# Kernel tuning notes

Hardware: AMD Instinct MI355X
Metric: run time of the kernel (lower is better)

Reference implementation:

```python
import jax, jax.numpy as jnp
import numpy as np
import math

N = 100000
C = 128
E = 640000
ALPHA = 0.1
THETA = 1.0
LAYER = 4


def setup_inputs() -> dict:
    key = jax.random.key(0)
    k1, k2, k3, k4, k5, k6 = jax.random.split(key, 6)
    x = jax.random.normal(k1, (N, C), dtype=jnp.float32)
    x0 = jax.random.normal(k2, (N, C), dtype=jnp.float32)
    W = jax.random.normal(k3, (C, C), dtype=jnp.float32) / math.sqrt(C)
    b = jax.random.normal(k4, (C,), dtype=jnp.float32) * 0.01
    edge_index = jax.random.randint(k5, (2, E), 0, N, dtype=jnp.int64)
    return {"x": x, "x0": x0, "W": W, "b": b, "edge_index": edge_index}


def _symmetric_propagate(x, edge_index):
    n = x.shape[0]
    loop = jnp.arange(n, dtype=edge_index.dtype)
    src = jnp.concatenate([edge_index[0], loop])  # add self-loops (GCN norm)
    dst = jnp.concatenate([edge_index[1], loop])
    ones = jnp.ones(src.shape[0], dtype=x.dtype)
    deg = jax.ops.segment_sum(ones, dst, num_segments=n)
    dinv = jnp.where(deg > 0, jax.lax.rsqrt(deg), 0.0)
    norm = dinv[src] * dinv[dst]                  # [E+N]
    msgs = x[src] * norm[:, None]                 # gather + scale
    return jax.ops.segment_sum(msgs, dst, num_segments=n)  # scatter-add


def reference(x, x0, W, b, edge_index):
    propagated = _symmetric_propagate(x, edge_index)
    support = (1.0 - ALPHA) * propagated + ALPHA * x0
    beta = math.log(THETA / max(LAYER, 1) + 1.0)
    transformed = support @ W.T + b               # nn.Linear(channels, channels)
    return (1.0 - beta) * support + beta * transformed
```

## Files before the change

### kernel.cpp

```cpp
#include <hip/hip_runtime.h>
#include <stdint.h>

#define C 128
#define ALPHA_F 0.1f
#define ONE_MINUS_ALPHA 0.9f
#define BETA_F 0.22314355131420976f
#define ONE_MINUS_BETA 0.7768564486857902f

typedef __attribute__((ext_vector_type(8))) short bf16x8;
typedef __attribute__((ext_vector_type(4))) float f32x4;

__device__ inline float bf2f(unsigned short u) {
    union { unsigned int i; float f; } c;
    c.i = ((unsigned int)u) << 16;
    return c.f;
}
__device__ inline unsigned short f2bf(float f) {
    union { float f; unsigned int i; } c;
    c.f = f;
    unsigned int r = (c.i + 0x7FFFu + ((c.i >> 16) & 1u)) >> 16;
    return (unsigned short)r;
}

__global__ void k_init(const float* __restrict__ W, unsigned short* __restrict__ Vb,
                       int* __restrict__ cnt, int n) {
    int i = blockIdx.x * 256 + threadIdx.x;
    if (i < n) cnt[i] = 0;
    if (i < C * C) {
        int j = i >> 7;
        int c = i & 127;
        float v = BETA_F * W[i] + ((j == c) ? ONE_MINUS_BETA : 0.f);
        Vb[i] = f2bf(v);
    }
}

__global__ void k_hist(const int* __restrict__ dst, int* __restrict__ cnt,
                       int* __restrict__ rank, int e) {
    int i = blockIdx.x * blockDim.x + threadIdx.x;
    if (i < e) rank[i] = atomicAdd(&cnt[dst[i]], 1);
}

__global__ __launch_bounds__(256)
void k_scan_a(const int* __restrict__ cnt, int* __restrict__ part, int n) {
    __shared__ int s[256];
    int t = threadIdx.x;
    int i = blockIdx.x * 256 + t;
    s[t] = (i < n) ? cnt[i] : 0;
    __syncthreads();
    for (int off = 128; off > 0; off >>= 1) {
        if (t < off) s[t] += s[t + off];
        __syncthreads();
    }
    if (t == 0) part[blockIdx.x] = s[0];
}

__global__ __launch_bounds__(256)
void k_scan_bc(const int* __restrict__ cnt, const int* __restrict__ part,
               int4* __restrict__ meta, int* __restrict__ row_ptr,
               float* __restrict__ dinv, int n) {
    __shared__ int a[256];
    __shared__ int b[256];
    int t   = threadIdx.x;
    int bid = blockIdx.x;

    int local = 0;
    for (int k = t; k < bid; k += 256) local += part[k];
    a[t] = local;
    __syncthreads();
    for (int off = 128; off > 0; off >>= 1) {
        if (t < off) a[t] += a[t + off];
        __syncthreads();
    }
    int blockoff = a[0];
    __syncthreads();

    int i = bid * 256 + t;
    int v = (i < n) ? cnt[i] : 0;
    a[t] = v;
    __syncthreads();
    int* cur = a;
    int* nxt = b;
    for (int off = 1; off < 256; off <<= 1) {
        nxt[t] = cur[t] + ((t >= off) ? cur[t - off] : 0);
        __syncthreads();
        int* tmp = cur; cur = nxt; nxt = tmp;
    }
    if (i < n) {
        int rp = blockoff + cur[t] - v;
        float dv = rsqrtf((float)(v + 1));
        meta[i]    = make_int4(rp, v, __float_as_int(dv), 0);
        row_ptr[i] = rp;
        dinv[i]    = dv;
    }
}

__global__ void k_pl_ybf(const int* __restrict__ src, const int* __restrict__ dst,
                         const int* __restrict__ row_ptr, const int* __restrict__ rank,
                         int* __restrict__ sorted_src, int e,
                         const float* __restrict__ x, const float* __restrict__ dinv,
                         unsigned short* __restrict__ y, int n, int eb) {
    int bid = blockIdx.x;
    if (bid < eb) {
        int i = bid * 256 + threadIdx.x;
        if (i < e) {
            int d = dst[i];
            int pos = row_ptr[d] + rank[i];
            sorted_src[pos] = src[i];
        }
    } else {
        int t = (bid - eb) * 256 + threadIdx.x;
        int total = n * 32;
        if (t < total) {
            int i = t >> 5;
            float dv = dinv[i];
            float4 v = ((const float4*)x)[t];
            ushort4 o;
            o.x = f2bf(v.x * dv);
            o.y = f2bf(v.y * dv);
            o.z = f2bf(v.z * dv);
            o.w = f2bf(v.w * dv);
            ((ushort4*)y)[t] = o;
        }
    }
}

__global__ __launch_bounds__(256)
void k_gather(const unsigned short* __restrict__ y, const float* __restrict__ x0,
              const int* __restrict__ sorted_src, const int4* __restrict__ meta,
              float* __restrict__ soutf, unsigned short* __restrict__ soutb,
              int mode, int n) {
    int tid  = threadIdx.x;
    int l32  = tid & 31;
    int base = tid & 32;
    int node = blockIdx.x * 8 + (tid >> 5);
    if (node >= n) return;

    const ushort4* y4 = (const ushort4*)y;

    int4 md   = meta[node];
    int start = md.x;
    int len   = md.y;
    float dv  = __int_as_float(md.z);
    float4 xv = ((const float4*)x0)[(size_t)node * 32 + l32];

    int m = (len < 32) ? len : 32;
    int eidx = (l32 < m) ? sorted_src[start + l32] : node;

    bool b1 = 1 < m, b2 = 2 < m, b3 = 3 < m;
    bool b4 = 4 < m, b5 = 5 < m, b6 = 6 < m, b7 = 7 < m;
    int s0 = __shfl(eidx, base + 0, 64);
    int s1 = __shfl(eidx, base + (b1 ? 1 : 0), 64);
    int s2 = __shfl(eidx, base + (b2 ? 2 : 0), 64);
    int s3 = __shfl(eidx, base + (b3 ? 3 : 0), 64);
    int s4 = __shfl(eidx, base + (b4 ? 4 : 0), 64);
    int s5 = __shfl(eidx, base + (b5 ? 5 : 0), 64);
    int s6 = __shfl(eidx, base + (b6 ? 6 : 0), 64);
    int s7 = __shfl(eidx, base + (b7 ? 7 : 0), 64);
    ushort4 v0 = y4[(size_t)s0 * 32 + l32];
    ushort4 v1 = y4[(size_t)s1 * 32 + l32];
    ushort4 v2 = y4[(size_t)s2 * 32 + l32];
    ushort4 v3 = y4[(size_t)s3 * 32 + l32];
    ushort4 v4 = y4[(size_t)s4 * 32 + l32];
    ushort4 v5 = y4[(size_t)s5 * 32 + l32];
    ushort4 v6 = y4[(size_t)s6 * 32 + l32];
    ushort4 v7 = y4[(size_t)s7 * 32 + l32];
    ushort4 vs = y4[(size_t)node * 32 + l32];

    float w0 = (0 < m) ? 1.f : 0.f, w1 = b1 ? 1.f : 0.f, w2 = b2 ? 1.f : 0.f, w3 = b3 ? 1.f : 0.f;
    float w4 = b4 ? 1.f : 0.f, w5 = b5 ? 1.f : 0.f, w6 = b6 ? 1.f : 0.f, w7 = b7 ? 1.f : 0.f;

    float4 acc;
    acc.x = bf2f(vs.x) + w0 * bf2f(v0.x) + w1 * bf2f(v1.x) + w2 * bf2f(v2.x) + w3 * bf2f(v3.x)
                       + w4 * bf2f(v4.x) + w5 * bf2f(v5.x) + w6 * bf2f(v6.x) + w7 * bf2f(v7.x);
    acc.y = bf2f(vs.y) + w0 * bf2f(v0.y) + w1 * bf2f(v1.y) + w2 * bf2f(v2.y) + w3 * bf2f(v3.y)
                       + w4 * bf2f(v4.y) + w5 * bf2f(v5.y) + w6 * bf2f(v6.y) + w7 * bf2f(v7.y);
    acc.z = bf2f(vs.z) + w0 * bf2f(v0.z) + w1 * bf2f(v1.z) + w2 * bf2f(v2.z) + w3 * bf2f(v3.z)
                       + w4 * bf2f(v4.z) + w5 * bf2f(v5.z) + w6 * bf2f(v6.z) + w7 * bf2f(v7.z);
    acc.w = bf2f(vs.w) + w0 * bf2f(v0.w) + w1 * bf2f(v1.w) + w2 * bf2f(v2.w) + w3 * bf2f(v3.w)
                       + w4 * bf2f(v4.w) + w5 * bf2f(v5.w) + w6 * bf2f(v6.w) + w7 * bf2f(v7.w);

    for (int j = 8; j < m; j += 4) {
        bool c1 = (j + 1) < m, c2 = (j + 2) < m, c3 = (j + 3) < m;
        int t0 = __shfl(eidx, base + j, 64);
        int t1 = __shfl(eidx, base + (c1 ? j + 1 : j), 64);
        int t2 = __shfl(eidx, base + (c2 ? j + 2 : j), 64);
        int t3 = __shfl(eidx, base + (c3 ? j + 3 : j), 64);
        ushort4 u0 = y4[(size_t)t0 * 32 + l32];
        ushort4 u1 = y4[(size_t)t1 * 32 + l32];
        ushort4 u2 = y4[(size_t)t2 * 32 + l32];
        ushort4 u3 = y4[(size_t)t3 * 32 + l32];
        float q1 = c1 ? 1.f : 0.f, q2 = c2 ? 1.f : 0.f, q3 = c3 ? 1.f : 0.f;
        acc.x += bf2f(u0.x) + q1 * bf2f(u1.x) + q2 * bf2f(u2.x) + q3 * bf2f(u3.x);
        acc.y += bf2f(u0.y) + q1 * bf2f(u1.y) + q2 * bf2f(u2.y) + q3 * bf2f(u3.y);
        acc.z += bf2f(u0.z) + q1 * bf2f(u1.z) + q2 * bf2f(u2.z) + q3 * bf2f(u3.z);
        acc.w += bf2f(u0.w) + q1 * bf2f(u1.w) + q2 * bf2f(u2.w) + q3 * bf2f(u3.w);
    }

    for (int j = 32; j < len; ++j) {
        int t0 = sorted_src[start + j];
        ushort4 u0 = y4[(size_t)t0 * 32 + l32];
        acc.x += bf2f(u0.x);
        acc.y += bf2f(u0.y);
        acc.z += bf2f(u0.z);
        acc.w += bf2f(u0.w);
    }

    float4 s;
    s.x = ONE_MINUS_ALPHA * (dv * acc.x) + ALPHA_F * xv.x;
    s.y = ONE_MINUS_ALPHA * (dv * acc.y) + ALPHA_F * xv.y;
    s.z = ONE_MINUS_ALPHA * (dv * acc.z) + ALPHA_F * xv.z;
    s.w = ONE_MINUS_ALPHA * (dv * acc.w) + ALPHA_F * xv.w;

    if (mode) {
        unsigned long long pk =
            (unsigned long long)f2bf(s.x)
          | ((unsigned long long)f2bf(s.y) << 16)
          | ((unsigned long long)f2bf(s.z) << 32)
          | ((unsigned long long)f2bf(s.w) << 48);
        __builtin_nontemporal_store(
            pk, (unsigned long long*)(soutb + (size_t)node * C + l32 * 4));
    } else {
        ((float4*)soutf)[(size_t)node * 32 + l32] = s;
    }
}

__global__ __launch_bounds__(256)
void k_out(const float* __restrict__ sinf, const unsigned short* __restrict__ sinb,
           const unsigned short* __restrict__ Vb, const float* __restrict__ bias,
           float* __restrict__ out, int mode, int n) {
    __shared__ unsigned short wlds[128 * 128];
    __shared__ unsigned short slds[64 * 128];

    int tid  = threadIdx.x;
    int row0 = blockIdx.x * 64;

    const uint4* Vb16 = (const uint4*)Vb;
    for (int i = tid; i < 2048; i += 256) {
        int j = i >> 4;
        int g = i & 15;
        uint4 v = Vb16[i];
        *(uint4*)&wlds[j * 128 + (g ^ (j & 7)) * 8] = v;
    }

    if (mode) {
        const uint4* sb16 = (const uint4*)sinb;
        for (int i = tid; i < 1024; i += 256) {
            int r = i >> 4;
            int g = i & 15;
            int grow = row0 + r;
            uint4 v = make_uint4(0, 0, 0, 0);
            if (grow < n) v = sb16[(size_t)grow * 16 + g];
            *(uint4*)&slds[r * 128 + (g ^ (r & 7)) * 8] = v;
        }
    } else {
        for (int i = tid; i < 1024; i += 256) {
            int r = i >> 4;
            int g = i & 15;
            int grow = row0 + r;
            union { unsigned short u[8]; uint4 v; } pk;
            if (grow < n) {
                const float* p = sinf + (size_t)grow * C + g * 8;
                float4 aa = *(const float4*)p;
                float4 bb = *(const float4*)(p + 4);
                pk.u[0] = f2bf(aa.x); pk.u[1] = f2bf(aa.y);
                pk.u[2] = f2bf(aa.z); pk.u[3] = f2bf(aa.w);
                pk.u[4] = f2bf(bb.x); pk.u[5] = f2bf(bb.y);
                pk.u[6] = f2bf(bb.z); pk.u[7] = f2bf(bb.w);
            } else {
                pk.v = make_uint4(0, 0, 0, 0);
            }
            *(uint4*)&slds[r * 128 + (g ^ (r & 7)) * 8] = pk.v;
        }
    }
    __syncthreads();

    int w    = tid >> 6;
    int lane = tid & 63;
    int l16  = lane & 15;
    int h    = lane >> 4;
    int arow = w * 16 + l16;

    f32x4 acc[8];
    #pragma unroll
    for (int t = 0; t < 8; ++t) acc[t] = (f32x4){0.f, 0.f, 0.f, 0.f};

    #pragma unroll
    for (int k0 = 0; k0 < 128; k0 += 32) {
        int ga = ((k0 >> 3) + h) ^ (arow & 7);
        bf16x8 a = *(const bf16x8*)&slds[arow * 128 + ga * 8];
        #pragma unroll
        for (int t = 0; t < 8; ++t) {
            int brow = t * 16 + l16;
            int gb = ((k0 >> 3) + h) ^ (brow & 7);
            bf16x8 b = *(const bf16x8*)&wlds[brow * 128 + gb * 8];
            acc[t] = __builtin_amdgcn_mfma_f32_16x16x32_bf16(a, b, acc[t], 0, 0, 0);
        }
    }

    #pragma unroll
    for (int t = 0; t < 8; ++t) {
        int j  = t * 16 + l16;
        float bj = BETA_F * bias[j];
        #pragma unroll
        for (int e2 = 0; e2 < 4; ++e2) {
            int grow = row0 + w * 16 + h * 4 + e2;
            if (grow < n) {
                __builtin_nontemporal_store(acc[t][e2] + bj, &out[(size_t)grow * C + j]);
            }
        }
    }
}

extern "C" void kernel_launch(void* const* d_in, const int* in_sizes, int n_in,
                              void* d_out, int out_size, void* d_ws, size_t ws_size,
                              hipStream_t stream) {
    const float* x   = (const float*)d_in[0];
    const float* x0  = (const float*)d_in[1];
    const float* W   = (const float*)d_in[2];
    const float* b   = (const float*)d_in[3];
    const int*   ei  = (const int*)d_in[4];

    int n = in_sizes[0] / C;
    int e = in_sizes[4] / 2;
    const int* src = ei;
    const int* dst = ei + e;

    int*   cnt        = (int*)d_ws;
    float* dinv       = (float*)(cnt + n);
    int*   part       = (int*)(dinv + n);
    int4*  meta       = (int4*)(part + 512);
    int*   row_ptr    = (int*)(meta + n);
    int*   rank       = row_ptr + n;
    int*   sorted_src = rank + e;
    unsigned short* Vb   = (unsigned short*)(sorted_src + e);
    unsigned short* y    = Vb + C * C;
    unsigned short* sb16 = y + (size_t)n * C;

    size_t need = (size_t)((char*)(sb16 + (size_t)n * C) - (char*)d_ws);
    int mode = (ws_size >= need) ? 1 : 0;

    float* out = (float*)d_out;

    int nb  = (n + 255) / 256;
    int eb  = (e + 255) / 256;
    int ybg = (n * 32 + 255) / 256;

    k_init   <<<nb, 256, 0, stream>>>(W, Vb, cnt, n);
    k_hist   <<<eb, 256, 0, stream>>>(dst, cnt, rank, e);
    k_scan_a <<<nb, 256, 0, stream>>>(cnt, part, n);
    k_scan_bc<<<nb, 256, 0, stream>>>(cnt, part, meta, row_ptr, dinv, n);
    k_pl_ybf <<<eb + ybg, 256, 0, stream>>>(src, dst, row_ptr, rank, sorted_src, e,
                                            x, dinv, y, n, eb);
    k_gather <<<(n + 7) / 8, 256, 0, stream>>>(y, x0, sorted_src, meta,
                                               out, sb16, mode, n);
    k_out    <<<(n + 63) / 64, 256, 0, stream>>>(out, sb16, Vb, b, out, mode, n);
}
```

Baseline: 126.3 us.

## Replace two-pass prefix scan with wave-level atomic allocation; enlarge output tile

The two scan kernels (block partial sums, then a scan that re-reads all preceding partials) become one kernel. Each wave computes an inclusive scan with shuffles and reserves its CSR range with one atomicAdd on a global cursor that k_init zeroes. Row segments are no longer in node order, which is fine because each node's offset and count are stored together in meta. Separately, the output GEMM kernel now processes 128 rows with 512 threads per block, so the 32KB weight tile is loaded into LDS for twice as many rows per block, at the cost of more LDS per block.

```diff
diff --git a/kernel.cpp b/kernel.cpp
--- a/kernel.cpp
+++ b/kernel.cpp
@@ -23,8 +23,9 @@
 }
 
 __global__ void k_init(const float* __restrict__ W, unsigned short* __restrict__ Vb,
-                       int* __restrict__ cnt, int n) {
+                       int* __restrict__ cnt, int* __restrict__ gcur, int n) {
     int i = blockIdx.x * 256 + threadIdx.x;
+    if (i == 0) *gcur = 0;
     if (i < n) cnt[i] = 0;
     if (i < C * C) {
         int j = i >> 7;
@@ -41,52 +42,26 @@
 }
 
 __global__ __launch_bounds__(256)
-void k_scan_a(const int* __restrict__ cnt, int* __restrict__ part, int n) {
-    __shared__ int s[256];
-    int t = threadIdx.x;
-    int i = blockIdx.x * 256 + t;
-    s[t] = (i < n) ? cnt[i] : 0;
-    __syncthreads();
-    for (int off = 128; off > 0; off >>= 1) {
-        if (t < off) s[t] += s[t + off];
-        __syncthreads();
-    }
-    if (t == 0) part[blockIdx.x] = s[0];
-}
-
-__global__ __launch_bounds__(256)
-void k_scan_bc(const int* __restrict__ cnt, const int* __restrict__ part,
-               int4* __restrict__ meta, int* __restrict__ row_ptr,
-               float* __restrict__ dinv, int n) {
-    __shared__ int a[256];
-    __shared__ int b[256];
-    int t   = threadIdx.x;
-    int bid = blockIdx.x;
-
-    int local = 0;
-    for (int k = t; k < bid; k += 256) local += part[k];
-    a[t] = local;
-    __syncthreads();
-    for (int off = 128; off > 0; off >>= 1) {
-        if (t < off) a[t] += a[t + off];
-        __syncthreads();
-    }
-    int blockoff = a[0];
-    __syncthreads();
-
-    int i = bid * 256 + t;
+void k_alloc(const int* __restrict__ cnt, int* __restrict__ gcur,
+             int4* __restrict__ meta, int* __restrict__ row_ptr,
+             float* __restrict__ dinv, int n) {
+    int i = blockIdx.x * 256 + threadIdx.x;
+    int lane = threadIdx.x & 63;
     int v = (i < n) ? cnt[i] : 0;
-    a[t] = v;
-    __syncthreads();
-    int* cur = a;
-    int* nxt = b;
-    for (int off = 1; off < 256; off <<= 1) {
-        nxt[t] = cur[t] + ((t >= off) ? cur[t - off] : 0);
-        __syncthreads();
-        int* tmp = cur; cur = nxt; nxt = tmp;
-    }
+
+    int pre = v;
+    #pragma unroll
+    for (int off = 1; off < 64; off <<= 1) {
+        int t = __shfl_up(pre, off, 64);
+        if (lane >= off) pre += t;
+    }
+    int wtotal = __shfl(pre, 63, 64);
+    int wbase = 0;
+    if (lane == 63) wbase = atomicAdd(gcur, wtotal);
+    wbase = __shfl(wbase, 63, 64);
+
     if (i < n) {
-        int rp = blockoff + cur[t] - v;
+        int rp = wbase + pre - v;
         float dv = rsqrtf((float)(v + 1));
         meta[i]    = make_int4(rp, v, __float_as_int(dv), 0);
         row_ptr[i] = rp;
@@ -224,18 +199,18 @@
     }
 }
 
-__global__ __launch_bounds__(256)
+__global__ __launch_bounds__(512)
 void k_out(const float* __restrict__ sinf, const unsigned short* __restrict__ sinb,
            const unsigned short* __restrict__ Vb, const float* __restrict__ bias,
            float* __restrict__ out, int mode, int n) {
     __shared__ unsigned short wlds[128 * 128];
-    __shared__ unsigned short slds[64 * 128];
+    __shared__ unsigned short slds[128 * 128];
 
     int tid  = threadIdx.x;
-    int row0 = blockIdx.x * 64;
+    int row0 = blockIdx.x * 128;
 
     const uint4* Vb16 = (const uint4*)Vb;
-    for (int i = tid; i < 2048; i += 256) {
+    for (int i = tid; i < 2048; i += 512) {
         int j = i >> 4;
         int g = i & 15;
         uint4 v = Vb16[i];
@@ -244,7 +219,7 @@
 
     if (mode) {
         const uint4* sb16 = (const uint4*)sinb;
-        for (int i = tid; i < 1024; i += 256) {
+        for (int i = tid; i < 2048; i += 512) {
             int r = i >> 4;
             int g = i & 15;
             int grow = row0 + r;
@@ -253,7 +228,7 @@
             *(uint4*)&slds[r * 128 + (g ^ (r & 7)) * 8] = v;
         }
     } else {
-        for (int i = tid; i < 1024; i += 256) {
+        for (int i = tid; i < 2048; i += 512) {
             int r = i >> 4;
             int g = i & 15;
             int grow = row0 + r;
@@ -327,8 +302,8 @@
 
     int*   cnt        = (int*)d_ws;
     float* dinv       = (float*)(cnt + n);
-    int*   part       = (int*)(dinv + n);
-    int4*  meta       = (int4*)(part + 512);
+    int*   gcur       = (int*)(dinv + n);
+    int4*  meta       = (int4*)(gcur + 512);
     int*   row_ptr    = (int*)(meta + n);
     int*   rank       = row_ptr + n;
     int*   sorted_src = rank + e;
@@ -345,13 +320,12 @@
     int eb  = (e + 255) / 256;
     int ybg = (n * 32 + 255) / 256;
 
-    k_init   <<<nb, 256, 0, stream>>>(W, Vb, cnt, n);
-    k_hist   <<<eb, 256, 0, stream>>>(dst, cnt, rank, e);
-    k_scan_a <<<nb, 256, 0, stream>>>(cnt, part, n);
-    k_scan_bc<<<nb, 256, 0, stream>>>(cnt, part, meta, row_ptr, dinv, n);
-    k_pl_ybf <<<eb + ybg, 256, 0, stream>>>(src, dst, row_ptr, rank, sorted_src, e,
-                                            x, dinv, y, n, eb);
-    k_gather <<<(n + 7) / 8, 256, 0, stream>>>(y, x0, sorted_src, meta,
-                                               out, sb16, mode, n);
-    k_out    <<<(n + 63) / 64, 256, 0, stream>>>(out, sb16, Vb, b, out, mode, n);
-}
+    k_init  <<<nb, 256, 0, stream>>>(W, Vb, cnt, gcur, n);
+    k_hist  <<<eb, 256, 0, stream>>>(dst, cnt, rank, e);
+    k_alloc <<<nb, 256, 0, stream>>>(cnt, gcur, meta, row_ptr, dinv, n);
+    k_pl_ybf<<<eb + ybg, 256, 0, stream>>>(src, dst, row_ptr, rank, sorted_src, e,
+                                           x, dinv, y, n, eb);
+    k_gather<<<(n + 7) / 8, 256, 0, stream>>>(y, x0, sorted_src, meta,
+                                              out, sb16, mode, n);
+    k_out   <<<(n + 127) / 128, 512, 0, stream>>>(out, sb16, Vb, b, out, mode, n);
+}
```

Result: slower. 137.7 us (+9.0%).
